# Optimization experiments

Measured on AMD Instinct MI355X. Metric: run time of the kernel, lower is better.

## Reference

```python
import jax, jax.numpy as jnp
import numpy as np

B, L, H = 4, 2048, 1024
NQ, NKV, D = 8, 2, 256
I, V = 3584, 16384
EPS = 1e-6
THETA = 1e7
ROPE_DIM = 64

def rmsnorm(x, w, eps=EPS):
    xf = x.astype(jnp.float32)
    rms = jax.lax.rsqrt(jnp.mean(xf * xf, axis=-1, keepdims=True) + eps)
    return (xf * rms).astype(x.dtype) * w

def apply_rope(x, positions):
    # x: [B, H, L, D]; rotate first ROPE_DIM dims, interleaved pairs
    n_pairs = ROPE_DIM // 2
    inv_freq = THETA ** (-2.0 * jnp.arange(n_pairs, dtype=jnp.float32) / ROPE_DIM)
    freqs = positions.astype(jnp.float32)[:, None] * inv_freq[None, :]  # [L, n_pairs]
    cos = jnp.cos(freqs)[None, None, :, :]
    sin = jnp.sin(freqs)[None, None, :, :]
    b, h, l, d = x.shape
    xr = x[..., :ROPE_DIM].reshape(b, h, l, n_pairs, 2)
    x0, x1 = xr[..., 0], xr[..., 1]
    r0 = x0 * cos - x1 * sin
    r1 = x0 * sin + x1 * cos
    rotated = jnp.stack([r0, r1], axis=-1).reshape(b, h, l, ROPE_DIM)
    return jnp.concatenate([rotated, x[..., ROPE_DIM:]], axis=-1)

def setup_inputs() -> dict:
    key = jax.random.key(0)
    ks = jax.random.split(key, 12)
    s = 0.02
    return {
        "embeddings": jax.random.normal(ks[0], (B, L, H), jnp.float32),
        "hidden_states": jax.random.normal(ks[1], (B, L, H), jnp.float32),
        "pre_emb_w": jnp.ones((H,), jnp.float32),
        "pre_hid_w": jnp.ones((H,), jnp.float32),
        "fc_w": jax.random.normal(ks[2], (H, 2 * H), jnp.float32) * s,
        "in_ln_w": jnp.ones((H,), jnp.float32),
        "q_w": jax.random.normal(ks[3], (2 * NQ * D, H), jnp.float32) * s,
        "k_w": jax.random.normal(ks[4], (NKV * D, H), jnp.float32) * s,
        "v_w": jax.random.normal(ks[5], (NKV * D, H), jnp.float32) * s,
        "o_w": jax.random.normal(ks[6], (H, NQ * D), jnp.float32) * s,
        "qn_w": jnp.ones((D,), jnp.float32),
        "kn_w": jnp.ones((D,), jnp.float32),
        "post_ln_w": jnp.ones((H,), jnp.float32),
        "gate_w": jax.random.normal(ks[7], (I, H), jnp.float32) * s,
        "up_w": jax.random.normal(ks[8], (I, H), jnp.float32) * s,
        "down_w": jax.random.normal(ks[9], (H, I), jnp.float32) * s,
        "norm_w": jnp.ones((H,), jnp.float32),
        "lm_w": jax.random.normal(ks[10], (V, H), jnp.float32) * s,
    }

def _attention(x, q_w, k_w, v_w, o_w, qn_w, kn_w):
    b, l, _ = x.shape
    qg = (x @ q_w.T).reshape(b, l, NQ, 2, D)
    q = qg[:, :, :, 0, :]
    gate = qg[:, :, :, 1, :]
    k = (x @ k_w.T).reshape(b, l, NKV, D)
    v = (x @ v_w.T).reshape(b, l, NKV, D)
    q = rmsnorm(q, qn_w)
    k = rmsnorm(k, kn_w)
    groups = NQ // NKV
    k = jnp.repeat(k, groups, axis=2)  # [B, L, NQ, D]
    v = jnp.repeat(v, groups, axis=2)
    q, k, v = (t.transpose(0, 2, 1, 3) for t in (q, k, v))  # [B, NQ, L, D]
    positions = jnp.arange(l)
    q = apply_rope(q, positions)
    k = apply_rope(k, positions)
    scores = jnp.einsum('bhqd,bhkd->bhqk', q, k) / jnp.sqrt(jnp.float32(D))
    causal = jnp.tril(jnp.ones((l, l), jnp.bool_))
    scores = jnp.where(causal[None, None], scores, jnp.finfo(scores.dtype).min)
    attn = jax.nn.softmax(scores, axis=-1)
    out = jnp.einsum('bhqk,bhkd->bhqd', attn, v)
    out = out.transpose(0, 2, 1, 3).reshape(b, l, NQ * D)
    out = out * jax.nn.sigmoid(gate.reshape(b, l, NQ * D))
    return out @ o_w.T

def reference(embeddings, hidden_states, pre_emb_w, pre_hid_w, fc_w, in_ln_w,
              q_w, k_w, v_w, o_w, qn_w, kn_w, post_ln_w, gate_w, up_w, down_w,
              norm_w, lm_w):
    x = jnp.concatenate([rmsnorm(embeddings, pre_emb_w),
                         rmsnorm(hidden_states, pre_hid_w)], axis=-1)
    x = x @ fc_w.T
    residual = x
    x = rmsnorm(x, in_ln_w)
    x = _attention(x, q_w, k_w, v_w, o_w, qn_w, kn_w)
    x = residual + x
    residual = x
    x = rmsnorm(x, post_ln_w)
    x = (jax.nn.silu(x @ gate_w.T) * (x @ up_w.T)) @ down_w.T
    x = residual + x
    x = rmsnorm(x, norm_w)
    return x @ lm_w.T
```

## Files before the change

### kernel.cpp

```cpp
#include <hip/hip_runtime.h>

typedef __bf16 bf16;
typedef __bf16 bf16x8 __attribute__((ext_vector_type(8)));
typedef __bf16 bf16x4 __attribute__((ext_vector_type(4)));
typedef float f32x4 __attribute__((ext_vector_type(4)));

__device__ inline f32x4 mfma16(bf16x8 a, bf16x8 b, f32x4 c) {
    return __builtin_amdgcn_mfma_f32_16x16x32_bf16(a, b, c, 0, 0, 0);
}

__device__ __forceinline__ void async_cp16(const void* g, void* l) {
    __builtin_amdgcn_global_load_lds(
        (__attribute__((address_space(1))) char*)g,
        (__attribute__((address_space(3))) char*)l,
        16, 0, 0);
}

__global__ __launch_bounds__(256) void w2b_kernel(const float* __restrict__ s,
                                                  bf16* __restrict__ d)
{
    const size_t i = ((size_t)blockIdx.x * 256 + threadIdx.x) * 4;
    const float4 f = *(const float4*)(s + i);
    bf16x4 t;
    t[0] = (bf16)f.x; t[1] = (bf16)f.y; t[2] = (bf16)f.z; t[3] = (bf16)f.w;
    *(bf16x4*)(d + i) = t;
}

__global__ __launch_bounds__(256) void w2b_qkv_kernel(
    const float* __restrict__ qw, const float* __restrict__ kw,
    const float* __restrict__ vw, bf16* __restrict__ dq)
{
    int bid = blockIdx.x;
    const float* s; bf16* d;
    if (bid < 4096)      { s = qw; d = dq; }
    else if (bid < 4608) { s = kw; d = dq + 4194304; bid -= 4096; }
    else                 { s = vw; d = dq + 4718592; bid -= 4608; }
    const size_t i = ((size_t)bid * 256 + threadIdx.x) * 4;
    const float4 f = *(const float4*)(s + i);
    bf16x4 t;
    t[0] = (bf16)f.x; t[1] = (bf16)f.y; t[2] = (bf16)f.z; t[3] = (bf16)f.w;
    *(bf16x4*)(d + i) = t;
}

__global__ __launch_bounds__(256) void w2b_gu_kernel(
    const float* __restrict__ gw, const float* __restrict__ uw, bf16* __restrict__ dg)
{
    int bid = blockIdx.x;
    const float* s; bf16* d;
    if (bid < 3584) { s = gw; d = dg; }
    else            { s = uw; d = dg + 3670016; bid -= 3584; }
    const size_t i = ((size_t)bid * 256 + threadIdx.x) * 4;
    const float4 f = *(const float4*)(s + i);
    bf16x4 t;
    t[0] = (bf16)f.x; t[1] = (bf16)f.y; t[2] = (bf16)f.z; t[3] = (bf16)f.w;
    *(bf16x4*)(d + i) = t;
}

template <int EPI>
__global__ __launch_bounds__(256) void gemm_kernel(
    const bf16* __restrict__ A, const bf16* __restrict__ B,
    const float* __restrict__ res, float* __restrict__ Cout,
    int M, int N, int K)
{
    __shared__ bf16 As[128][64];
    __shared__ bf16 Bs[128][64];
    const int tid = threadIdx.x;
    const int wave = tid >> 6, lane = tid & 63;
    const int quad = lane >> 4, l16 = lane & 15;
    const int xsw = l16 & 7;

    const int nby = M >> 7, nbx = N >> 7;
    const int nwg = nbx * nby;
    int bid = blockIdx.x;
    {
        const int q = nwg >> 3, r = nwg & 7;
        const int x = bid & 7, loc = bid >> 3;
        bid = (x < r ? x * (q + 1) : r * (q + 1) + (x - r) * q) + loc;
    }
    const int pg = nbx << 3;
    const int g = bid / pg, rem = bid - g * pg;
    const int by = (g << 3) + (rem & 7);
    const int bx = rem >> 3;
    const int row0 = by << 7, col0 = bx << 7;
    const int wrow = ((wave >> 1) << 6), wcol = ((wave & 1) << 6);

    f32x4 acc[4][4] = {};

    const int srow = tid >> 3;
    const int scol = ((tid & 7) ^ (srow & 7)) * 8;
    const bf16* Ag = A + (size_t)(row0 + srow) * K + scol;
    const bf16* Bg = B + (size_t)(col0 + srow) * K + scol;
    const size_t K32 = (size_t)32 * K;

    for (int kb = 0; kb < K; kb += 64) {
#pragma unroll
        for (int q = 0; q < 4; ++q) {
            async_cp16(Ag + q * K32 + kb, &As[0][0] + q * 2048 + wave * 512);
            async_cp16(Bg + q * K32 + kb, &Bs[0][0] + q * 2048 + wave * 512);
        }
        __syncthreads();
        bf16x8 af[8], bfr[8];
#pragma unroll
        for (int i = 0; i < 4; ++i) {
            af[i * 2 + 0] = *(const bf16x8*)(&As[wrow + i * 16 + l16][(quad ^ xsw) * 8]);
            af[i * 2 + 1] = *(const bf16x8*)(&As[wrow + i * 16 + l16][((4 + quad) ^ xsw) * 8]);
        }
#pragma unroll
        for (int j = 0; j < 4; ++j) {
            bfr[j * 2 + 0] = *(const bf16x8*)(&Bs[wcol + j * 16 + l16][(quad ^ xsw) * 8]);
            bfr[j * 2 + 1] = *(const bf16x8*)(&Bs[wcol + j * 16 + l16][((4 + quad) ^ xsw) * 8]);
        }
#pragma unroll
        for (int i = 0; i < 4; ++i)
#pragma unroll
            for (int j = 0; j < 4; ++j) {
                acc[i][j] = mfma16(af[i * 2 + 0], bfr[j * 2 + 0], acc[i][j]);
                acc[i][j] = mfma16(af[i * 2 + 1], bfr[j * 2 + 1], acc[i][j]);
            }
        __syncthreads();
    }

#pragma unroll
    for (int i = 0; i < 4; ++i) {
        const int row = row0 + wrow + i * 16 + quad * 4;
#pragma unroll
        for (int j = 0; j < 4; ++j) {
            const int col = col0 + wcol + j * 16 + l16;
#pragma unroll
            for (int r = 0; r < 4; ++r) {
                const size_t idx = (size_t)(row + r) * N + col;
                float v = acc[i][j][r];
                if (EPI == 1) Cout[idx] = v + res[idx];
                else          Cout[idx] = v;
            }
        }
    }
}

template <int EPI>
__global__ __launch_bounds__(512, 2) void gemm256_kernel(
    const bf16* __restrict__ A, const bf16* __restrict__ B,
    const float* __restrict__ res, float* __restrict__ Cout,
    bf16* __restrict__ hout, int M, int N, int K)
{
    __shared__ bf16 As[2][2][128][64];
    __shared__ bf16 Bs[2][2][128][64];
    const int tid = threadIdx.x;
    const int wid = tid >> 6, lane = tid & 63;
    const int quad = lane >> 4, l16 = lane & 15;
    const int wm = wid >> 2, wn = wid & 3;
    const int xsw = l16 & 7;
    const int bofs = (wn & 1) * 64;

    const int nby = M >> 8, nbx = N >> 8;
    const int nwg = nbx * nby;
    int bid = blockIdx.x;
    {
        const int q = nwg >> 3, r = nwg & 7;
        const int x = bid & 7, loc = bid >> 3;
        bid = (x < r ? x * (q + 1) : r * (q + 1) + (x - r) * q) + loc;
    }
    const int pg = nbx << 3;
    const int g = bid / pg, rem = bid - g * pg;
    const int by = (g << 3) + (rem & 7);
    const int bx = rem >> 3;
    const int row0 = by << 8, col0 = bx << 8;

    const int srow = tid >> 3;
    const int scol = ((tid & 7) ^ ((tid >> 3) & 7)) * 8;
    const bf16* Abase = A + (size_t)(row0 + srow) * K + scol;
    const bf16* Bbase = B + (size_t)(col0 + srow) * K + scol;
    const size_t K64 = (size_t)K * 64;
    const size_t K128 = (size_t)K * 128;

    f32x4 acc[8][4] = {};
    bf16x8 af[8], bf0[4], bf1[4];

#define STG_A(BUF, HH, KB) do { \
    const bf16* _g = Abase + (size_t)(HH) * K128 + (KB); \
    bf16* _l = &As[BUF][HH][0][0] + wid * 512; \
    async_cp16(_g, _l); \
    async_cp16(_g + K64, _l + 4096); } while (0)
#define STG_B(BUF, HH, KB) do { \
    const bf16* _g = Bbase + (size_t)(HH) * K128 + (KB); \
    bf16* _l = &Bs[BUF][HH][0][0] + wid * 512; \
    async_cp16(_g, _l); \
    async_cp16(_g + K64, _l + 4096); } while (0)

#define RD_A(BUF, RH) do { \
    const bf16 (*Ah_)[64] = As[BUF][wm]; \
    _Pragma("unroll") for (int f = 0; f < 4; ++f) { \
        af[f*2+0] = *(const bf16x8*)(&Ah_[(RH)*64 + f*16 + l16][(quad ^ xsw) * 8]); \
        af[f*2+1] = *(const bf16x8*)(&Ah_[(RH)*64 + f*16 + l16][((4 + quad) ^ xsw) * 8]); } } while (0)

#define RD_B(BUF, CH, BF) do { \
    const bf16 (*Bh_)[64] = Bs[BUF][wn >> 1]; \
    _Pragma("unroll") for (int f = 0; f < 2; ++f) { \
        BF[f*2+0] = *(const bf16x8*)(&Bh_[bofs + (CH)*32 + f*16 + l16][(quad ^ xsw) * 8]); \
        BF[f*2+1] = *(const bf16x8*)(&Bh_[bofs + (CH)*32 + f*16 + l16][((4 + quad) ^ xsw) * 8]); } } while (0)

#define MFMA_Q(RH, CH, BF) do { \
    _Pragma("unroll") for (int f = 0; f < 4; ++f) \
    _Pragma("unroll") for (int f2 = 0; f2 < 2; ++f2) { \
        acc[(RH)*4+f][(CH)*2+f2] = mfma16(af[f*2+0], BF[f2*2+0], acc[(RH)*4+f][(CH)*2+f2]); \
        acc[(RH)*4+f][(CH)*2+f2] = mfma16(af[f*2+1], BF[f2*2+1], acc[(RH)*4+f][(CH)*2+f2]); } } while (0)

    const int NT = K >> 6;
    STG_A(0, 0, 0); STG_A(0, 1, 0); STG_B(0, 0, 0); STG_B(0, 1, 0);
    if (NT > 1) {
        STG_A(1, 0, 64); STG_A(1, 1, 64); STG_B(1, 0, 64); STG_B(1, 1, 64);
        asm volatile("s_waitcnt vmcnt(8)" ::: "memory");
    } else {
        asm volatile("s_waitcnt vmcnt(0)" ::: "memory");
    }
    __builtin_amdgcn_sched_barrier(0);
    __builtin_amdgcn_s_barrier();
    RD_A(0, 0); RD_B(0, 0, bf0); RD_B(0, 1, bf1);
    __builtin_amdgcn_sched_barrier(0);

    for (int t = 0; t < NT; ++t) {
        const int c = t & 1, n = c ^ 1;
        const int kb1 = (t + 1) << 6, kb2 = (t + 2) << 6;
        if (t >= 1 && t + 1 < NT) { STG_A(n, 0, kb1); STG_A(n, 1, kb1); }
        asm volatile("s_waitcnt lgkmcnt(4)" ::: "memory");
        __builtin_amdgcn_sched_barrier(0);
        __builtin_amdgcn_s_setprio(1);
        MFMA_Q(0, 0, bf0);
        __builtin_amdgcn_s_setprio(0);
        asm volatile("s_waitcnt lgkmcnt(0)" ::: "memory");
        __builtin_amdgcn_sched_barrier(0);
        __builtin_amdgcn_s_setprio(1);
        MFMA_Q(0, 1, bf1);
        __builtin_amdgcn_s_setprio(0);
        RD_A(c, 1);
        __builtin_amdgcn_sched_barrier(0);
        __builtin_amdgcn_s_barrier();
        if (t + 2 < NT) { STG_B(c, 0, kb2); STG_B(c, 1, kb2); }
        asm volatile("s_waitcnt lgkmcnt(0)" ::: "memory");
        __builtin_amdgcn_sched_barrier(0);
        __builtin_amdgcn_s_setprio(1);
        MFMA_Q(1, 0, bf0);
        MFMA_Q(1, 1, bf1);
        __builtin_amdgcn_s_setprio(0);
        if (t + 1 < NT) {
            if (t + 2 < NT) { asm volatile("s_waitcnt vmcnt(4)" ::: "memory"); }
            else            { asm volatile("s_waitcnt vmcnt(0)" ::: "memory"); }
            __builtin_amdgcn_sched_barrier(0);
            RD_A(n, 0); RD_B(n, 0, bf0); RD_B(n, 1, bf1);
            __builtin_amdgcn_sched_barrier(0);
        }
        __builtin_amdgcn_s_barrier();
    }
#undef STG_A
#undef STG_B
#undef RD_A
#undef RD_B
#undef MFMA_Q

#pragma unroll
    for (int fr = 0; fr < 8; ++fr) {
        const int row = row0 + wm * 128 + fr * 16 + quad * 4;
#pragma unroll
        for (int fc = 0; fc < 4; ++fc) {
            const int col = col0 + wn * 64 + fc * 16 + l16;
#pragma unroll
            for (int r = 0; r < 4; ++r) {
                const size_t idx = (size_t)(row + r) * N + col;
                float v = acc[fr][fc][r];
                if (EPI == 1) {
                    Cout[idx] = v + res[idx];
                } else if (EPI == 2) {
                    const float gg = res[idx];
                    hout[idx] = (bf16)(gg * (1.f / (1.f + __expf(-gg))) * v);
                } else {
                    Cout[idx] = v;
                }
            }
        }
    }
}

__global__ __launch_bounds__(256) void prenorm_kernel(
    const float* __restrict__ emb, const float* __restrict__ hid,
    const float* __restrict__ we, const float* __restrict__ wh,
    bf16* __restrict__ xcat)
{
    const int rr = blockIdx.x * 4 + (threadIdx.x >> 6);
    const int lane = threadIdx.x & 63;
    const int half = rr & 1, row = rr >> 1;
    const float* x = (half ? hid : emb) + (size_t)row * 1024;
    const float* w = half ? wh : we;
    float4 v[4]; float ss = 0.f;
#pragma unroll
    for (int j = 0; j < 4; ++j) {
        v[j] = *(const float4*)(x + (size_t)(lane + 64 * j) * 4);
        ss += v[j].x * v[j].x + v[j].y * v[j].y + v[j].z * v[j].z + v[j].w * v[j].w;
    }
#pragma unroll
    for (int m = 32; m; m >>= 1) ss += __shfl_xor(ss, m, 64);
    const float rms = rsqrtf(ss * (1.f / 1024.f) + 1e-6f);
    bf16* o = xcat + (size_t)row * 2048 + half * 1024;
#pragma unroll
    for (int j = 0; j < 4; ++j) {
        const int d = (lane + 64 * j) * 4;
        float4 wv = *(const float4*)(w + d);
        bf16x4 t;
        t[0] = (bf16)(v[j].x * rms * wv.x);
        t[1] = (bf16)(v[j].y * rms * wv.y);
        t[2] = (bf16)(v[j].z * rms * wv.z);
        t[3] = (bf16)(v[j].w * rms * wv.w);
        *(bf16x4*)(o + d) = t;
    }
}

__global__ __launch_bounds__(256) void rmsnorm_kernel(
    const float* __restrict__ xin, const float* __restrict__ w, bf16* __restrict__ out)
{
    const int row = blockIdx.x * 4 + (threadIdx.x >> 6);
    const int lane = threadIdx.x & 63;
    const float* x = xin + (size_t)row * 1024;
    float4 v[4]; float ss = 0.f;
#pragma unroll
    for (int j = 0; j < 4; ++j) {
        v[j] = *(const float4*)(x + (size_t)(lane + 64 * j) * 4);
        ss += v[j].x * v[j].x + v[j].y * v[j].y + v[j].z * v[j].z + v[j].w * v[j].w;
    }
#pragma unroll
    for (int m = 32; m; m >>= 1) ss += __shfl_xor(ss, m, 64);
    const float rms = rsqrtf(ss * (1.f / 1024.f) + 1e-6f);
    bf16* o = out + (size_t)row * 1024;
#pragma unroll
    for (int j = 0; j < 4; ++j) {
        const int d = (lane + 64 * j) * 4;
        float4 wv = *(const float4*)(w + d);
        bf16x4 t;
        t[0] = (bf16)(v[j].x * rms * wv.x);
        t[1] = (bf16)(v[j].y * rms * wv.y);
        t[2] = (bf16)(v[j].z * rms * wv.z);
        t[3] = (bf16)(v[j].w * rms * wv.w);
        *(bf16x4*)(o + d) = t;
    }
}

__global__ __launch_bounds__(256) void qprep_kernel(
    const float* __restrict__ qg, const float* __restrict__ qn_w, bf16* __restrict__ qa)
{
    const int row = blockIdx.x * 4 + (threadIdx.x >> 6);
    const int lane = threadIdx.x & 63;
    const int h = row & 7, bl = row >> 3;
    const int l = bl & 2047, b = bl >> 11;
    const float* x = qg + (size_t)row * 512;
    float4 v = *(const float4*)(x + lane * 4);
    float ss = v.x * v.x + v.y * v.y + v.z * v.z + v.w * v.w;
#pragma unroll
    for (int m = 32; m; m >>= 1) ss += __shfl_xor(ss, m, 64);
    const float rms = rsqrtf(ss * (1.f / 256.f) + 1e-6f);
    const float4 wv = *(const float4*)(qn_w + lane * 4);
    float y0 = v.x * rms * wv.x, y1 = v.y * rms * wv.y;
    float y2 = v.z * rms * wv.z, y3 = v.w * rms * wv.w;
    if (lane < 16) {
        const float inv0 = powf(1e7f, -(float)(4 * lane) * (1.f / 64.f));
        const float inv1 = powf(1e7f, -(float)(4 * lane + 2) * (1.f / 64.f));
        const float a0 = (float)l * inv0, a1 = (float)l * inv1;
        const float c0 = cosf(a0), s0 = sinf(a0), c1 = cosf(a1), s1 = sinf(a1);
        const float r0 = y0 * c0 - y1 * s0, r1 = y0 * s0 + y1 * c0;
        const float r2 = y2 * c1 - y3 * s1, r3 = y2 * s1 + y3 * c1;
        y0 = r0; y1 = r1; y2 = r2; y3 = r3;
    }
    bf16* o = qa + ((size_t)((b * 8 + h) * 2048 + l)) * 256 + lane * 4;
    bf16x4 t;
    t[0] = (bf16)(y0 * 0.0625f); t[1] = (bf16)(y1 * 0.0625f);
    t[2] = (bf16)(y2 * 0.0625f); t[3] = (bf16)(y3 * 0.0625f);
    *(bf16x4*)o = t;
}

__global__ __launch_bounds__(256) void kprep_kernel(
    const float* __restrict__ kvf, const float* __restrict__ kn_w, bf16* __restrict__ ka)
{
    const int row = blockIdx.x * 4 + (threadIdx.x >> 6);
    const int lane = threadIdx.x & 63;
    const int kv = row & 1, bl = row >> 1;
    const int l = bl & 2047, b = bl >> 11;
    const float* x = kvf + (size_t)bl * 1024 + kv * 256;
    float4 v = *(const float4*)(x + lane * 4);
    float ss = v.x * v.x + v.y * v.y + v.z * v.z + v.w * v.w;
#pragma unroll
    for (int m = 32; m; m >>= 1) ss += __shfl_xor(ss, m, 64);
    const float rms = rsqrtf(ss * (1.f / 256.f) + 1e-6f);
    const float4 wv = *(const float4*)(kn_w + lane * 4);
    float y0 = v.x * rms * wv.x, y1 = v.y * rms * wv.y;
    float y2 = v.z * rms * wv.z, y3 = v.w * rms * wv.w;
    if (lane < 16) {
        const float inv0 = powf(1e7f, -(float)(4 * lane) * (1.f / 64.f));
        const float inv1 = powf(1e7f, -(float)(4 * lane + 2) * (1.f / 64.f));
        const float a0 = (float)l * inv0, a1 = (float)l * inv1;
        const float c0 = cosf(a0), s0 = sinf(a0), c1 = cosf(a1), s1 = sinf(a1);
        const float r0 = y0 * c0 - y1 * s0, r1 = y0 * s0 + y1 * c0;
        const float r2 = y2 * c1 - y3 * s1, r3 = y2 * s1 + y3 * c1;
        y0 = r0; y1 = r1; y2 = r2; y3 = r3;
    }
    bf16* o = ka + ((size_t)((b * 2 + kv) * 2048 + l)) * 256 + lane * 4;
    bf16x4 t;
    t[0] = (bf16)y0; t[1] = (bf16)y1; t[2] = (bf16)y2; t[3] = (bf16)y3;
    *(bf16x4*)o = t;
}

__global__ __launch_bounds__(256) void vprep_kernel(const float* __restrict__ kvf,
                                                    bf16* __restrict__ vt)
{
    __shared__ float t[64][65];
    const int l0 = blockIdx.x << 6;
    const int d0 = blockIdx.y << 6;
    const int b = blockIdx.z >> 1, kv = blockIdx.z & 1;
    const int tx = threadIdx.x & 63, ty = threadIdx.x >> 6;
    const float* src = kvf + (size_t)b * 2048 * 1024 + 512 + kv * 256;
#pragma unroll
    for (int j = 0; j < 16; ++j) {
        const int l = ty + j * 4;
        t[l][tx] = src[(size_t)(l0 + l) * 1024 + d0 + tx];
    }
    __syncthreads();
    bf16* dst = vt + (size_t)(b * 2 + kv) * 256 * 2048;
#pragma unroll
    for (int j = 0; j < 16; ++j) {
        const int d = ty + j * 4;
        dst[(size_t)(d0 + d) * 2048 + l0 + tx] = (bf16)t[tx][d];
    }
}

__global__ __launch_bounds__(256) void attn_kernel(
    const bf16* __restrict__ qa, const bf16* __restrict__ ka,
    const bf16* __restrict__ vt, const float* __restrict__ qg,
    bf16* __restrict__ ag)
{
    __shared__ bf16 Ks[32 * 264];
    __shared__ bf16 Vt[256 * 40];
    __shared__ bf16 Pw[4 * 16 * 40];
    const int tid = threadIdx.x;
    const int wave = tid >> 6, lane = tid & 63;
    const int quad = lane >> 4, l16 = lane & 15;
    const int bid = blockIdx.x;
    const int j = bid & 15, h = (bid >> 4) & 7, b = bid >> 7;
    const int kvh = h >> 2;
    const bf16* qptr = qa + ((size_t)(b * 8 + h)) * 2048 * 256;
    const bf16* kptr = ka + ((size_t)(b * 2 + kvh)) * 2048 * 256;
    const bf16* vptr = vt + ((size_t)(b * 2 + kvh)) * 256 * 2048;

    for (int s = 0; s < 2; ++s) {
        const int qt = s ? (31 - j) : j;
        const int qbase = qt * 64 + wave * 16;

        bf16x8 qf[8];
#pragma unroll
        for (int db = 0; db < 8; ++db)
            qf[db] = *(const bf16x8*)(qptr + (size_t)(qbase + l16) * 256 + db * 32 + quad * 8);

        f32x4 o_acc[16] = {};
        float m_i[4], l_i[4];
#pragma unroll
        for (int r = 0; r < 4; ++r) { m_i[r] = -1e30f; l_i[r] = 0.f; }

        const int ntiles = qt * 2 + 2;
        for (int kt = 0; kt < ntiles; ++kt) {
            const int kvs = kt * 32;
#pragma unroll
            for (int c = 0; c < 4; ++c) {
                const int idx = tid + c * 256;
                const int kr = idx >> 5, kc = (idx & 31) * 8;
                *(bf16x8*)(&Ks[kr * 264 + kc]) = *(const bf16x8*)(kptr + (size_t)(kvs + kr) * 256 + kc);
                const int vd = idx >> 2, vc = (idx & 3) * 8;
                *(bf16x8*)(&Vt[vd * 40 + vc]) = *(const bf16x8*)(vptr + (size_t)vd * 2048 + kvs + vc);
            }
            __syncthreads();

            f32x4 s0 = {}, s1 = {};
#pragma unroll
            for (int db = 0; db < 8; ++db) {
                bf16x8 k0 = *(const bf16x8*)(&Ks[l16 * 264 + db * 32 + quad * 8]);
                bf16x8 k1 = *(const bf16x8*)(&Ks[(16 + l16) * 264 + db * 32 + quad * 8]);
                s0 = mfma16(qf[db], k0, s0);
                s1 = mfma16(qf[db], k1, s1);
            }

            float alpha[4], p0v[4], p1v[4];
#pragma unroll
            for (int r = 0; r < 4; ++r) {
                const int qrow = qbase + quad * 4 + r;
                float a0 = (kvs + l16 > qrow) ? -1e30f : s0[r];
                float a1 = (kvs + 16 + l16 > qrow) ? -1e30f : s1[r];
                float mx = fmaxf(a0, a1);
#pragma unroll
                for (int m = 8; m; m >>= 1) mx = fmaxf(mx, __shfl_xor(mx, m, 64));
                const float mnew = fmaxf(m_i[r], mx);
                const float a = __expf(m_i[r] - mnew);
                const float p0 = __expf(a0 - mnew);
                const float p1 = __expf(a1 - mnew);
                float ps = p0 + p1;
#pragma unroll
                for (int m = 8; m; m >>= 1) ps += __shfl_xor(ps, m, 64);
                l_i[r] = l_i[r] * a + ps;
                m_i[r] = mnew;
                alpha[r] = a; p0v[r] = p0; p1v[r] = p1;
            }
#pragma unroll
            for (int t = 0; t < 16; ++t) {
                f32x4 o = o_acc[t];
                o[0] *= alpha[0]; o[1] *= alpha[1]; o[2] *= alpha[2]; o[3] *= alpha[3];
                o_acc[t] = o;
            }
            bf16* pw = &Pw[wave * 16 * 40];
#pragma unroll
            for (int r = 0; r < 4; ++r) {
                pw[(quad * 4 + r) * 40 + l16]      = (bf16)p0v[r];
                pw[(quad * 4 + r) * 40 + 16 + l16] = (bf16)p1v[r];
            }
            __syncthreads();
            const bf16x8 pa = *(const bf16x8*)(&pw[l16 * 40 + quad * 8]);
#pragma unroll
            for (int t = 0; t < 16; ++t) {
                bf16x8 vfr = *(const bf16x8*)(&Vt[(t * 16 + l16) * 40 + quad * 8]);
                o_acc[t] = mfma16(pa, vfr, o_acc[t]);
            }
            __syncthreads();
        }

#pragma unroll
        for (int r = 0; r < 4; ++r) {
            const float inv = 1.f / l_i[r];
            const int row = qbase + quad * 4 + r;
            const float* gr = qg + ((size_t)((b * 2048 + row) * 8 + h)) * 512 + 256;
            bf16* ar = ag + ((size_t)(b * 2048 + row)) * 2048 + h * 256;
#pragma unroll
            for (int t = 0; t < 16; ++t) {
                const int d = t * 16 + l16;
                const float o = o_acc[t][r] * inv;
                const float gg = gr[d];
                ar[d] = (bf16)(o * (1.f / (1.f + __expf(-gg))));
            }
        }
    }
}

extern "C" void kernel_launch(void* const* d_in, const int* in_sizes, int n_in,
                              void* d_out, int out_size, void* d_ws, size_t ws_size,
                              hipStream_t stream)
{
    const float* emb       = (const float*)d_in[0];
    const float* hid       = (const float*)d_in[1];
    const float* pre_emb_w = (const float*)d_in[2];
    const float* pre_hid_w = (const float*)d_in[3];
    const float* fc_w      = (const float*)d_in[4];
    const float* in_ln_w   = (const float*)d_in[5];
    const float* q_w       = (const float*)d_in[6];
    const float* k_w       = (const float*)d_in[7];
    const float* v_w       = (const float*)d_in[8];
    const float* o_w       = (const float*)d_in[9];
    const float* qn_w      = (const float*)d_in[10];
    const float* kn_w      = (const float*)d_in[11];
    const float* post_ln_w = (const float*)d_in[12];
    const float* gate_w    = (const float*)d_in[13];
    const float* up_w      = (const float*)d_in[14];
    const float* down_w    = (const float*)d_in[15];
    const float* norm_w    = (const float*)d_in[16];
    const float* lm_w      = (const float*)d_in[17];
    float* out = (float*)d_out;
    char* ws = (char*)d_ws;

    float* xres = (float*)(ws + 0);
    bf16*  xln  = (bf16*)(ws + 33554432);
    char*  C    = ws + 50331648;
    char*  D    = ws + 184549376;
    char*  E    = ws + 318767104;
    float* qg   = (float*)C;
    float* gf   = (float*)C;
    bf16*  xcat = (bf16*)D;
    float* kvf  = (float*)(D + 33554432);
    bf16*  ag   = (bf16*)(D + 67108864);
    bf16*  qa   = (bf16*)E;
    bf16*  ka   = (bf16*)(E + 33554432);
    bf16*  va   = (bf16*)(E + 41943040);
    bf16*  hb   = (bf16*)E;
    bf16*  wbC  = (bf16*)C;
    bf16*  wbD  = (bf16*)D;
    bf16*  wkv  = (bf16*)D + 4194304;
    bf16*  wbDt = (bf16*)(D + 117440512);

    prenorm_kernel<<<4096, 256, 0, stream>>>(emb, hid, pre_emb_w, pre_hid_w, xcat);

    w2b_kernel<<<2048, 256, 0, stream>>>(fc_w, wbC);
    gemm_kernel<0><<<512, 256, 0, stream>>>(xcat, wbC, nullptr, xres, 8192, 1024, 2048);
    rmsnorm_kernel<<<2048, 256, 0, stream>>>(xres, in_ln_w, xln);

    w2b_qkv_kernel<<<5120, 256, 0, stream>>>(q_w, k_w, v_w, wbD);
    gemm256_kernel<0><<<512, 512, 0, stream>>>(xln, wbD, nullptr, qg, nullptr, 8192, 4096, 1024);
    gemm_kernel<0><<<512, 256, 0, stream>>>(xln, wkv, nullptr, kvf, 8192, 1024, 1024);

    qprep_kernel<<<16384, 256, 0, stream>>>(qg, qn_w, qa);
    kprep_kernel<<<4096, 256, 0, stream>>>(kvf, kn_w, ka);
    vprep_kernel<<<dim3(32, 4, 8), 256, 0, stream>>>(kvf, va);
    attn_kernel<<<512, 256, 0, stream>>>(qa, ka, va, qg, ag);

    w2b_kernel<<<2048, 256, 0, stream>>>(o_w, wbC);
    gemm_kernel<1><<<512, 256, 0, stream>>>(ag, wbC, xres, xres, 8192, 1024, 2048);
    rmsnorm_kernel<<<2048, 256, 0, stream>>>(xres, post_ln_w, xln);

    w2b_gu_kernel<<<7168, 256, 0, stream>>>(gate_w, up_w, wbDt);
    gemm256_kernel<0><<<448, 512, 0, stream>>>(xln, wbDt, nullptr, gf, nullptr, 8192, 3584, 1024);
    gemm256_kernel<2><<<448, 512, 0, stream>>>(xln, wbDt + 3670016, gf, nullptr, hb, 8192, 3584, 1024);

    w2b_kernel<<<3584, 256, 0, stream>>>(down_w, wbC);
    gemm_kernel<1><<<512, 256, 0, stream>>>(hb, wbC, xres, xres, 8192, 1024, 3584);
    rmsnorm_kernel<<<2048, 256, 0, stream>>>(xres, norm_w, xln);

    w2b_kernel<<<16384, 256, 0, stream>>>(lm_w, wbC);
    gemm256_kernel<0><<<2048, 512, 0, stream>>>(xln, wbC, nullptr, out, nullptr, 8192, 16384, 1024);
}
```

Measured before the change: 1.728 ms.

## Double-buffer GEMM LDS tiles and XOR-swizzle attention K tile

The GEMM kernel now uses two LDS buffers per operand and issues the async global-to-LDS loads for the next K-tile before computing on the current one. This overlaps memory latency with MFMA work and removes one barrier per iteration, at the cost of doubled LDS use (64KB), which may lower occupancy. The attention kernel replaces padded K/V/P shared arrays with unpadded ones, applying an XOR swizzle to the K tile and dropping padding on Vt and Pw, which may add bank conflicts there.

```diff
diff --git a/kernel.cpp b/kernel.cpp
--- a/kernel.cpp
+++ b/kernel.cpp
@@ -62,8 +62,8 @@
     const float* __restrict__ res, float* __restrict__ Cout,
     int M, int N, int K)
 {
-    __shared__ bf16 As[128][64];
-    __shared__ bf16 Bs[128][64];
+    __shared__ bf16 As[2][128][64];
+    __shared__ bf16 Bs[2][128][64];
     const int tid = threadIdx.x;
     const int wave = tid >> 6, lane = tid & 63;
     const int quad = lane >> 4, l16 = lane & 15;
@@ -92,23 +92,27 @@
     const bf16* Bg = B + (size_t)(col0 + srow) * K + scol;
     const size_t K32 = (size_t)32 * K;
 
-    for (int kb = 0; kb < K; kb += 64) {
-#pragma unroll
-        for (int q = 0; q < 4; ++q) {
-            async_cp16(Ag + q * K32 + kb, &As[0][0] + q * 2048 + wave * 512);
-            async_cp16(Bg + q * K32 + kb, &Bs[0][0] + q * 2048 + wave * 512);
+#define STG128(BUF, KB) do { \
+    _Pragma("unroll") for (int q = 0; q < 4; ++q) { \
+        async_cp16(Ag + q * K32 + (KB), &As[BUF][0][0] + q * 2048 + wave * 512); \
+        async_cp16(Bg + q * K32 + (KB), &Bs[BUF][0][0] + q * 2048 + wave * 512); } } while (0)
+
+    const int NT = K >> 6;
+    STG128(0, 0);
+    __syncthreads();
+    for (int t = 0; t < NT; ++t) {
+        const int c = t & 1, n = c ^ 1;
+        if (t + 1 < NT) STG128(n, (t + 1) * 64);
+        bf16x8 af[8], bfr[8];
+#pragma unroll
+        for (int i = 0; i < 4; ++i) {
+            af[i * 2 + 0] = *(const bf16x8*)(&As[c][wrow + i * 16 + l16][(quad ^ xsw) * 8]);
+            af[i * 2 + 1] = *(const bf16x8*)(&As[c][wrow + i * 16 + l16][((4 + quad) ^ xsw) * 8]);
         }
-        __syncthreads();
-        bf16x8 af[8], bfr[8];
-#pragma unroll
-        for (int i = 0; i < 4; ++i) {
-            af[i * 2 + 0] = *(const bf16x8*)(&As[wrow + i * 16 + l16][(quad ^ xsw) * 8]);
-            af[i * 2 + 1] = *(const bf16x8*)(&As[wrow + i * 16 + l16][((4 + quad) ^ xsw) * 8]);
-        }
 #pragma unroll
         for (int j = 0; j < 4; ++j) {
-            bfr[j * 2 + 0] = *(const bf16x8*)(&Bs[wcol + j * 16 + l16][(quad ^ xsw) * 8]);
-            bfr[j * 2 + 1] = *(const bf16x8*)(&Bs[wcol + j * 16 + l16][((4 + quad) ^ xsw) * 8]);
+            bfr[j * 2 + 0] = *(const bf16x8*)(&Bs[c][wcol + j * 16 + l16][(quad ^ xsw) * 8]);
+            bfr[j * 2 + 1] = *(const bf16x8*)(&Bs[c][wcol + j * 16 + l16][((4 + quad) ^ xsw) * 8]);
         }
 #pragma unroll
         for (int i = 0; i < 4; ++i)
@@ -119,6 +123,7 @@
             }
         __syncthreads();
     }
+#undef STG128
 
 #pragma unroll
     for (int i = 0; i < 4; ++i) {
@@ -433,9 +438,9 @@
     const bf16* __restrict__ vt, const float* __restrict__ qg,
     bf16* __restrict__ ag)
 {
-    __shared__ bf16 Ks[32 * 264];
-    __shared__ bf16 Vt[256 * 40];
-    __shared__ bf16 Pw[4 * 16 * 40];
+    __shared__ bf16 Ks[32 * 256];
+    __shared__ bf16 Vt[256 * 32];
+    __shared__ bf16 Pw[4 * 16 * 32];
     const int tid = threadIdx.x;
     const int wave = tid >> 6, lane = tid & 63;
     const int quad = lane >> 4, l16 = lane & 15;
@@ -466,18 +471,20 @@
 #pragma unroll
             for (int c = 0; c < 4; ++c) {
                 const int idx = tid + c * 256;
-                const int kr = idx >> 5, kc = (idx & 31) * 8;
-                *(bf16x8*)(&Ks[kr * 264 + kc]) = *(const bf16x8*)(kptr + (size_t)(kvs + kr) * 256 + kc);
+                const int kr = idx >> 5, kc32 = idx & 31;
+                *(bf16x8*)(&Ks[kr * 256 + (kc32 ^ (kr & 7)) * 8]) =
+                    *(const bf16x8*)(kptr + (size_t)(kvs + kr) * 256 + kc32 * 8);
                 const int vd = idx >> 2, vc = (idx & 3) * 8;
-                *(bf16x8*)(&Vt[vd * 40 + vc]) = *(const bf16x8*)(vptr + (size_t)vd * 2048 + kvs + vc);
+                *(bf16x8*)(&Vt[vd * 32 + vc]) = *(const bf16x8*)(vptr + (size_t)vd * 2048 + kvs + vc);
             }
             __syncthreads();
 
             f32x4 s0 = {}, s1 = {};
 #pragma unroll
             for (int db = 0; db < 8; ++db) {
-                bf16x8 k0 = *(const bf16x8*)(&Ks[l16 * 264 + db * 32 + quad * 8]);
-                bf16x8 k1 = *(const bf16x8*)(&Ks[(16 + l16) * 264 + db * 32 + quad * 8]);
+                const int ch = (db * 4 + quad) ^ (l16 & 7);
+                bf16x8 k0 = *(const bf16x8*)(&Ks[l16 * 256 + ch * 8]);
+                bf16x8 k1 = *(const bf16x8*)(&Ks[(16 + l16) * 256 + ch * 8]);
                 s0 = mfma16(qf[db], k0, s0);
                 s1 = mfma16(qf[db], k1, s1);
             }
@@ -508,17 +515,17 @@
                 o[0] *= alpha[0]; o[1] *= alpha[1]; o[2] *= alpha[2]; o[3] *= alpha[3];
                 o_acc[t] = o;
             }
-            bf16* pw = &Pw[wave * 16 * 40];
+            bf16* pw = &Pw[wave * 16 * 32];
 #pragma unroll
             for (int r = 0; r < 4; ++r) {
-                pw[(quad * 4 + r) * 40 + l16]      = (bf16)p0v[r];
-                pw[(quad * 4 + r) * 40 + 16 + l16] = (bf16)p1v[r];
+                pw[(quad * 4 + r) * 32 + l16]      = (bf16)p0v[r];
+                pw[(quad * 4 + r) * 32 + 16 + l16] = (bf16)p1v[r];
             }
             __syncthreads();
-            const bf16x8 pa = *(const bf16x8*)(&pw[l16 * 40 + quad * 8]);
+            const bf16x8 pa = *(const bf16x8*)(&pw[l16 * 32 + quad * 8]);
 #pragma unroll
             for (int t = 0; t < 16; ++t) {
-                bf16x8 vfr = *(const bf16x8*)(&Vt[(t * 16 + l16) * 40 + quad * 8]);
+                bf16x8 vfr = *(const bf16x8*)(&Vt[(t * 16 + l16) * 32 + quad * 8]);
                 o_acc[t] = mfma16(pa, vfr, o_acc[t]);
             }
             __syncthreads();
```

Measured after the change: 1.710 ms. No clear change (-1.1%).
